# Kernel optimization log

Measured on AMD Instinct MI355X. Metric: run time of the kernel, lower is better.

Reference implementation:

```python
import jax, jax.numpy as jnp
import numpy as np

N_EMITTERS = 200000
N_FRAMES = 500


def setup_inputs() -> dict:
    key = jax.random.key(0)
    k1, _ = jax.random.split(key)
    # initial state must be one-hot per emitter: column 0 = 'on', column 1 = 'off'
    on = jax.random.bernoulli(k1, 0.5, (N_EMITTERS,))
    initial = jnp.stack([on, ~on], axis=-1).astype(jnp.float32)  # [N, 2] one-hot
    # transition[j] is the categorical distribution over {stay-ish, flip-ish} given row j
    transition = jnp.array([[0.5, 0.5], [0.9, 0.1]], dtype=jnp.float32)
    # transition_matrix[0] = identity (keep state), transition_matrix[1] = swap (flip state)
    transition_matrix = jnp.array([[[1.0, 0.0], [0.0, 1.0]],
                                   [[0.0, 1.0], [1.0, 0.0]]], dtype=jnp.float32)
    return {"initial": initial, "transition": transition,
            "transition_matrix": transition_matrix, "n_frames": N_FRAMES}


def reference(initial, transition, transition_matrix, n_frames):
    # Faithful translation of the per-frame Python loop as a single lax.scan.
    # Original: A = Cat(transition).sample([N]) -> A[n, j] ~ Cat(transition[j, :]) in {0, 1}
    #           t = (state * A).sum(-1)   (selects A at the current one-hot state index)
    #           state = state @ transition_matrix[t]
    # Output: per-frame on-mask (original returned np.where(state[:, 0] == 1) indices,
    # which has data-dependent shape; we return the equivalent dense mask).
    p1 = transition[:, 1]  # prob of drawing class 1 for each of the 2 row-distributions
    keys = jax.random.split(jax.random.key(42), n_frames)

    def step(state, k):
        u = jax.random.uniform(k, (state.shape[0], 2), dtype=state.dtype)  # [N, 2]
        A = (u < p1[None, :]).astype(state.dtype)  # categorical sample per row dist, {0,1}
        t = jnp.sum(state * A, axis=-1).astype(jnp.int32)  # [N] chosen action per emitter
        m = transition_matrix[t]  # [N, 2, 2] identity-or-swap
        new_state = jnp.einsum('ni,nij->nj', state, m)  # [N, 2] one-hot update
        return new_state, new_state[:, 0]

    _, on_mask = jax.lax.scan(step, initial, keys)
    return on_mask  # [n_frames, N], 1.0 where emitter is in the 'on' state
```

## Files before the change

kernel.cpp:

```cpp
#include <hip/hip_runtime.h>
#include <stdint.h>


#define ROTL32(x, d) __builtin_amdgcn_alignbit((x), (x), 32 - (d))

__device__ __forceinline__ void tf2x32(uint32_t k0, uint32_t k1,
                                       uint32_t x0, uint32_t x1,
                                       uint32_t& o0, uint32_t& o1) {
  const uint32_t k2 = k0 ^ k1 ^ 0x1BD11BDAu;
  x0 += k0; x1 += k1;
#define TF_R(d) { x0 += x1; x1 = ROTL32(x1, d) ^ x0; }
  TF_R(13) TF_R(15) TF_R(26) TF_R(6)
  x0 += k1; x1 += k2 + 1u;
  TF_R(17) TF_R(29) TF_R(16) TF_R(24)
  x0 += k2; x1 += k0 + 2u;
  TF_R(13) TF_R(15) TF_R(26) TF_R(6)
  x0 += k0; x1 += k1 + 3u;
  TF_R(17) TF_R(29) TF_R(16) TF_R(24)
  x0 += k1; x1 += k2 + 4u;
  TF_R(13) TF_R(15) TF_R(26) TF_R(6)
  x0 += k2; x1 += k0 + 5u;
#undef TF_R
  o0 = x0; o1 = x1;
}

__global__ void subkeys_kernel(uint2* __restrict__ ks, int nf, int cap) {
  const int f = blockIdx.x * blockDim.x + threadIdx.x;
  if (f < nf) {
    uint32_t a, b;
    tf2x32(0u, 42u, 0u, (uint32_t)f, a, b);
    ks[f] = make_uint2(a, b);
  } else if (f < cap) {
    ks[f] = make_uint2(0u, 0u);
  }
}

__device__ __forceinline__ uint32_t cipher(uint32_t k0, uint32_t k1,
                                           uint32_t k2, uint32_t c1,
                                           uint32_t c2, uint32_t c3,
                                           uint32_t c4, uint32_t c5,
                                           uint32_t x1in) {
  uint32_t x0 = k0 + x1in;
  uint32_t x1 = ROTL32(x1in, 13) ^ x0;
  x0 += x1; x1 = ROTL32(x1, 15) ^ x0;
  x0 += x1; x1 = ROTL32(x1, 26) ^ x0;
  x0 += x1; x1 = ROTL32(x1,  6) ^ x0;
  x1 += c1; x0 = x0 + k1 + x1;
  x1 = ROTL32(x1, 17) ^ x0;
  x0 += x1; x1 = ROTL32(x1, 29) ^ x0;
  x0 += x1; x1 = ROTL32(x1, 16) ^ x0;
  x0 += x1; x1 = ROTL32(x1, 24) ^ x0;
  x1 += c2; x0 = x0 + k2 + x1;
  x1 = ROTL32(x1, 13) ^ x0;
  x0 += x1; x1 = ROTL32(x1, 15) ^ x0;
  x0 += x1; x1 = ROTL32(x1, 26) ^ x0;
  x0 += x1; x1 = ROTL32(x1,  6) ^ x0;
  x1 += c3; x0 = x0 + k0 + x1;
  x1 = ROTL32(x1, 17) ^ x0;
  x0 += x1; x1 = ROTL32(x1, 29) ^ x0;
  x0 += x1; x1 = ROTL32(x1, 16) ^ x0;
  x0 += x1; x1 = ROTL32(x1, 24) ^ x0;
  x1 += c4; x0 = x0 + k1 + x1;
  x1 = ROTL32(x1, 13) ^ x0;
  x0 += x1; x1 = ROTL32(x1, 15) ^ x0;
  x0 += x1; x1 = ROTL32(x1, 26) ^ x0;
  x0 += x1; x1 = ROTL32(x1,  6) ^ x0;
  return (x0 + k2) ^ (x1 + c5);
}

template <int NC>
__device__ __forceinline__ void run_nc(
    const uint2* __restrict__ ks, float* __restrict__ out,
    const uint32_t* __restrict__ base, const int* __restrict__ noff,
    uint32_t* __restrict__ s, int N, int nf,
    uint32_t tsh0, uint32_t tsh1, uint32_t sw0, uint32_t sw1) {
  uint32_t thr[NC];
#pragma unroll
  for (int j = 0; j < NC; ++j) thr[j] = s[j] ? tsh1 : tsh0;

  const int ng = nf / 4;
  for (int g = 0; g < ng; ++g) {
    const int f0 = 4 * g;
    uint2 k[4];
#pragma unroll
    for (int i = 0; i < 4; ++i) k[i] = ks[f0 + i];

    uint32_t vals[4][NC];
#pragma unroll
    for (int i = 0; i < 4; ++i) {
      const uint32_t k0 = k[i].x, k1 = k[i].y;
      const uint32_t k2 = k0 ^ k1 ^ 0x1BD11BDAu;
      const uint32_t c1 = k2 + 1u, c2 = k0 + 2u, c3 = k1 + 3u,
                     c4 = k2 + 4u, c5 = k0 + 5u;
#pragma unroll
      for (int j = 0; j < NC; ++j) {
        const uint32_t r = cipher(k0, k1, k2, c1, c2, c3, c4, c5,
                                  base[j] + s[j] + k1);
        s[j] ^= (r < thr[j]) ? sw1 : sw0;
        thr[j] = s[j] ? tsh1 : tsh0;
        vals[i][j] = s[j] ? 0u : 0x3f800000u;
      }
    }
#pragma unroll
    for (int i = 0; i < 4; ++i) {
      uint32_t* row = (uint32_t*)out + (size_t)(f0 + i) * N;
#pragma unroll
      for (int j = 0; j < NC; ++j)
        __builtin_nontemporal_store(vals[i][j], row + noff[j]);
    }
  }
  for (int f = ng * 4; f < nf; ++f) {
    const uint2 kk = ks[f];
    const uint32_t k0 = kk.x, k1 = kk.y;
    const uint32_t k2 = k0 ^ k1 ^ 0x1BD11BDAu;
    const uint32_t c1 = k2 + 1u, c2 = k0 + 2u, c3 = k1 + 3u,
                   c4 = k2 + 4u, c5 = k0 + 5u;
    uint32_t* row = (uint32_t*)out + (size_t)f * N;
#pragma unroll
    for (int j = 0; j < NC; ++j) {
      const uint32_t r = cipher(k0, k1, k2, c1, c2, c3, c4, c5,
                                base[j] + s[j] + k1);
      s[j] ^= (r < thr[j]) ? sw1 : sw0;
      thr[j] = s[j] ? tsh1 : tsh0;
      __builtin_nontemporal_store(s[j] ? 0u : 0x3f800000u, row + noff[j]);
    }
  }
}

__device__ __forceinline__ void get_params(
    const float* transition, const float* tmat,
    uint32_t& tsh0, uint32_t& tsh1, uint32_t& sw0, uint32_t& sw1) {
  const uint64_t t0w = ((uint64_t)(uint32_t)ceilf(transition[1] * 8388608.0f)) << 9;
  const uint64_t t1w = ((uint64_t)(uint32_t)ceilf(transition[3] * 8388608.0f)) << 9;
  tsh0 = (t0w > 0xFFFFFFFFull) ? 0xFFFFFFFFu : (uint32_t)t0w;
  tsh1 = (t1w > 0xFFFFFFFFull) ? 0xFFFFFFFFu : (uint32_t)t1w;
  sw0 = (tmat[1] != 0.0f) ? 1u : 0u;
  sw1 = (tmat[5] != 0.0f) ? 1u : 0u;
}

__global__ __launch_bounds__(256) void markov3_kernel(
    const float* __restrict__ initial, const float* __restrict__ transition,
    const float* __restrict__ tmat, const uint2* __restrict__ ks,
    float* __restrict__ out, int N, int nf, int T, int extra) {
  const int t = blockIdx.x * blockDim.x + threadIdx.x;

  uint32_t tsh0, tsh1, sw0, sw1;
  get_params(transition, tmat, tsh0, tsh1, sw0, sw1);

  const int n0 = 3 * t;
  uint32_t s[4];
  uint32_t base[4];
  int noff[4];
#pragma unroll
  for (int j = 0; j < 3; ++j) {
    const int n = n0 + j;
    s[j] = (initial[2 * n] != 0.0f) ? 0u : 1u;
    base[j] = 2u * (uint32_t)n;
    noff[j] = n;
  }
  if (t < extra) {
    const int n3 = 3 * T + t;
    s[3] = (initial[2 * n3] != 0.0f) ? 0u : 1u;
    base[3] = 2u * (uint32_t)n3;
    noff[3] = n3;
    run_nc<4>(ks, out, base, noff, s, N, nf, tsh0, tsh1, sw0, sw1);
  } else {
    run_nc<3>(ks, out, base, noff, s, N, nf, tsh0, tsh1, sw0, sw1);
  }
}

__global__ __launch_bounds__(256) void markov_generic_kernel(
    const float* __restrict__ initial, const float* __restrict__ transition,
    const float* __restrict__ tmat, const uint2* __restrict__ ks,
    float* __restrict__ out, int N, int nf) {
  const int n = blockIdx.x * blockDim.x + threadIdx.x;
  if (n >= N) return;
  uint32_t tsh0, tsh1, sw0, sw1;
  get_params(transition, tmat, tsh0, tsh1, sw0, sw1);
  uint32_t s[1] = {(initial[2 * n] != 0.0f) ? 0u : 1u};
  uint32_t base[1] = {2u * (uint32_t)n};
  int noff[1] = {n};
  run_nc<1>(ks, out, base, noff, s, N, nf, tsh0, tsh1, sw0, sw1);
}

__global__ __launch_bounds__(256) void markov_lds_kernel(
    const float* __restrict__ initial, const float* __restrict__ transition,
    const float* __restrict__ tmat, float* __restrict__ out,
    int N, int nf, int cap) {
  extern __shared__ uint2 kf[];
  for (int f = threadIdx.x; f < cap; f += blockDim.x) {
    uint2 k = make_uint2(0u, 0u);
    if (f < nf) {
      uint32_t a, b;
      tf2x32(0u, 42u, 0u, (uint32_t)f, a, b);
      k = make_uint2(a, b);
    }
    kf[f] = k;
  }
  __syncthreads();
  const int n = blockIdx.x * blockDim.x + threadIdx.x;
  if (n >= N) return;
  uint32_t tsh0, tsh1, sw0, sw1;
  get_params(transition, tmat, tsh0, tsh1, sw0, sw1);
  uint32_t s[1] = {(initial[2 * n] != 0.0f) ? 0u : 1u};
  uint32_t base[1] = {2u * (uint32_t)n};
  int noff[1] = {n};
  run_nc<1>(kf, out, base, noff, s, N, nf, tsh0, tsh1, sw0, sw1);
}

extern "C" void kernel_launch(void* const* d_in, const int* in_sizes, int n_in,
                              void* d_out, int out_size, void* d_ws, size_t ws_size,
                              hipStream_t stream) {
  const float* initial    = (const float*)d_in[0];
  const float* transition = (const float*)d_in[1];
  const float* tmat       = (const float*)d_in[2];
  float* out = (float*)d_out;

  const int N  = in_sizes[0] / 2;
  const int nf = (N > 0) ? (out_size / N) : 0;
  if (N <= 0 || nf <= 0) return;

  const int cap = ((nf + 3) / 4 + 1) * 4;
  const size_t need = (size_t)cap * sizeof(uint2);

  if (ws_size < need) {
    const int block = 256;
    const int grid = (N + block - 1) / block;
    markov_lds_kernel<<<grid, block, need, stream>>>(initial, transition,
                                                     tmat, out, N, nf, cap);
    return;
  }

  uint2* ks = (uint2*)d_ws;
  subkeys_kernel<<<(cap + 255) / 256, 256, 0, stream>>>(ks, nf, cap);

  const int T = 65536;
  if (N >= 3 * T && N < 4 * T) {
    const int extra = N - 3 * T;
    markov3_kernel<<<T / 256, 256, 0, stream>>>(initial, transition, tmat,
                                                ks, out, N, nf, T, extra);
  } else {
    const int block = 256;
    const int grid = (N + block - 1) / block;
    markov_generic_kernel<<<grid, block, 0, stream>>>(initial, transition,
                                                      tmat, ks, out, N, nf);
  }
}
```

Measured before the change: 276.1 us.

## Stage 16-frame output tiles in LDS and write 128-bit nontemporal stores

Replaces the 3-4 emitters-per-thread kernel with a one-emitter-per-thread kernel. Each thread computes 16 frames into a double-buffered LDS tile, and the block then transposes the tile so each lane writes four contiguous floats with a 128-bit nontemporal store. The aim is to cut store instruction count and improve write coalescing for the 400 MB output. In exchange it adds a __syncthreads per 16 frames and LDS traffic, and it changes the parallelism from 65536 threads with 3 emitters each to 200000 threads with 1 each.

```diff
diff --git a/kernel.cpp b/kernel.cpp
--- a/kernel.cpp
+++ b/kernel.cpp
@@ -3,6 +3,8 @@
 
 
 #define ROTL32(x, d) __builtin_amdgcn_alignbit((x), (x), 32 - (d))
+
+typedef uint32_t v4u __attribute__((ext_vector_type(4)));
 
 __device__ __forceinline__ void tf2x32(uint32_t k0, uint32_t k1,
                                        uint32_t x0, uint32_t x1,
@@ -68,65 +70,6 @@
   return (x0 + k2) ^ (x1 + c5);
 }
 
-template <int NC>
-__device__ __forceinline__ void run_nc(
-    const uint2* __restrict__ ks, float* __restrict__ out,
-    const uint32_t* __restrict__ base, const int* __restrict__ noff,
-    uint32_t* __restrict__ s, int N, int nf,
-    uint32_t tsh0, uint32_t tsh1, uint32_t sw0, uint32_t sw1) {
-  uint32_t thr[NC];
-#pragma unroll
-  for (int j = 0; j < NC; ++j) thr[j] = s[j] ? tsh1 : tsh0;
-
-  const int ng = nf / 4;
-  for (int g = 0; g < ng; ++g) {
-    const int f0 = 4 * g;
-    uint2 k[4];
-#pragma unroll
-    for (int i = 0; i < 4; ++i) k[i] = ks[f0 + i];
-
-    uint32_t vals[4][NC];
-#pragma unroll
-    for (int i = 0; i < 4; ++i) {
-      const uint32_t k0 = k[i].x, k1 = k[i].y;
-      const uint32_t k2 = k0 ^ k1 ^ 0x1BD11BDAu;
-      const uint32_t c1 = k2 + 1u, c2 = k0 + 2u, c3 = k1 + 3u,
-                     c4 = k2 + 4u, c5 = k0 + 5u;
-#pragma unroll
-      for (int j = 0; j < NC; ++j) {
-        const uint32_t r = cipher(k0, k1, k2, c1, c2, c3, c4, c5,
-                                  base[j] + s[j] + k1);
-        s[j] ^= (r < thr[j]) ? sw1 : sw0;
-        thr[j] = s[j] ? tsh1 : tsh0;
-        vals[i][j] = s[j] ? 0u : 0x3f800000u;
-      }
-    }
-#pragma unroll
-    for (int i = 0; i < 4; ++i) {
-      uint32_t* row = (uint32_t*)out + (size_t)(f0 + i) * N;
-#pragma unroll
-      for (int j = 0; j < NC; ++j)
-        __builtin_nontemporal_store(vals[i][j], row + noff[j]);
-    }
-  }
-  for (int f = ng * 4; f < nf; ++f) {
-    const uint2 kk = ks[f];
-    const uint32_t k0 = kk.x, k1 = kk.y;
-    const uint32_t k2 = k0 ^ k1 ^ 0x1BD11BDAu;
-    const uint32_t c1 = k2 + 1u, c2 = k0 + 2u, c3 = k1 + 3u,
-                   c4 = k2 + 4u, c5 = k0 + 5u;
-    uint32_t* row = (uint32_t*)out + (size_t)f * N;
-#pragma unroll
-    for (int j = 0; j < NC; ++j) {
-      const uint32_t r = cipher(k0, k1, k2, c1, c2, c3, c4, c5,
-                                base[j] + s[j] + k1);
-      s[j] ^= (r < thr[j]) ? sw1 : sw0;
-      thr[j] = s[j] ? tsh1 : tsh0;
-      __builtin_nontemporal_store(s[j] ? 0u : 0x3f800000u, row + noff[j]);
-    }
-  }
-}
-
 __device__ __forceinline__ void get_params(
     const float* transition, const float* tmat,
     uint32_t& tsh0, uint32_t& tsh1, uint32_t& sw0, uint32_t& sw1) {
@@ -138,34 +81,76 @@
   sw1 = (tmat[5] != 0.0f) ? 1u : 0u;
 }
 
-__global__ __launch_bounds__(256) void markov3_kernel(
+__global__ __launch_bounds__(256) void markov_t_kernel(
     const float* __restrict__ initial, const float* __restrict__ transition,
     const float* __restrict__ tmat, const uint2* __restrict__ ks,
-    float* __restrict__ out, int N, int nf, int T, int extra) {
-  const int t = blockIdx.x * blockDim.x + threadIdx.x;
+    float* __restrict__ out, int N, int nf) {
+  __shared__ uint32_t buf[2][16 * 256];
+
+  const int t = (int)threadIdx.x;
+  const int n0b = (int)blockIdx.x * 256;
+  const int n = n0b + t;
+  const int rem = N - n0b;
+  const int valid = rem < 256 ? rem : 256;
+  const bool active = (t < valid);
 
   uint32_t tsh0, tsh1, sw0, sw1;
   get_params(transition, tmat, tsh0, tsh1, sw0, sw1);
 
-  const int n0 = 3 * t;
-  uint32_t s[4];
-  uint32_t base[4];
-  int noff[4];
+  uint32_t s = 0u, thr = tsh0, base = 0u;
+  if (active) {
+    s = (initial[2 * n] != 0.0f) ? 0u : 1u;
+    thr = s ? tsh1 : tsh0;
+    base = 2u * (uint32_t)n;
+  }
+
+  const int w = t >> 6, l = t & 63;
+  const int e0 = 4 * l;
+
+  const int ng = nf / 16;
+  for (int g = 0; g < ng; ++g) {
+    const int f0 = g * 16;
+    uint32_t* b = buf[g & 1];
+    if (active) {
 #pragma unroll
-  for (int j = 0; j < 3; ++j) {
-    const int n = n0 + j;
-    s[j] = (initial[2 * n] != 0.0f) ? 0u : 1u;
-    base[j] = 2u * (uint32_t)n;
-    noff[j] = n;
-  }
-  if (t < extra) {
-    const int n3 = 3 * T + t;
-    s[3] = (initial[2 * n3] != 0.0f) ? 0u : 1u;
-    base[3] = 2u * (uint32_t)n3;
-    noff[3] = n3;
-    run_nc<4>(ks, out, base, noff, s, N, nf, tsh0, tsh1, sw0, sw1);
-  } else {
-    run_nc<3>(ks, out, base, noff, s, N, nf, tsh0, tsh1, sw0, sw1);
+      for (int i = 0; i < 16; ++i) {
+        const uint2 kk = ks[f0 + i];
+        const uint32_t k0 = kk.x, k1 = kk.y;
+        const uint32_t k2 = k0 ^ k1 ^ 0x1BD11BDAu;
+        const uint32_t c1 = k2 + 1u, c2 = k0 + 2u, c3 = k1 + 3u,
+                       c4 = k2 + 4u, c5 = k0 + 5u;
+        const uint32_t r = cipher(k0, k1, k2, c1, c2, c3, c4, c5,
+                                  base + s + k1);
+        s ^= (r < thr) ? sw1 : sw0;
+        thr = s ? tsh1 : tsh0;
+        b[i * 256 + t] = s ? 0u : 0x3f800000u;
+      }
+    }
+    __syncthreads();
+    if (e0 < valid) {
+#pragma unroll
+      for (int c = 0; c < 4; ++c) {
+        const int r = 4 * w + c;
+        const v4u v = *(const v4u*)&b[r * 256 + e0];
+        __builtin_nontemporal_store(
+            v, (v4u*)(out + (size_t)(f0 + r) * N + (n0b + e0)));
+      }
+    }
+  }
+  for (int f = ng * 16; f < nf; ++f) {
+    if (active) {
+      const uint2 kk = ks[f];
+      const uint32_t k0 = kk.x, k1 = kk.y;
+      const uint32_t k2 = k0 ^ k1 ^ 0x1BD11BDAu;
+      const uint32_t c1 = k2 + 1u, c2 = k0 + 2u, c3 = k1 + 3u,
+                     c4 = k2 + 4u, c5 = k0 + 5u;
+      const uint32_t r = cipher(k0, k1, k2, c1, c2, c3, c4, c5,
+                                base + s + k1);
+      s ^= (r < thr) ? sw1 : sw0;
+      thr = s ? tsh1 : tsh0;
+      __builtin_nontemporal_store(s ? 0u : 0x3f800000u,
+                                  (uint32_t*)(out + (size_t)f * N) + n);
+    }
   }
 }
 
@@ -177,10 +162,21 @@
   if (n >= N) return;
   uint32_t tsh0, tsh1, sw0, sw1;
   get_params(transition, tmat, tsh0, tsh1, sw0, sw1);
-  uint32_t s[1] = {(initial[2 * n] != 0.0f) ? 0u : 1u};
-  uint32_t base[1] = {2u * (uint32_t)n};
-  int noff[1] = {n};
-  run_nc<1>(ks, out, base, noff, s, N, nf, tsh0, tsh1, sw0, sw1);
+  uint32_t s = (initial[2 * n] != 0.0f) ? 0u : 1u;
+  uint32_t thr = s ? tsh1 : tsh0;
+  const uint32_t base = 2u * (uint32_t)n;
+  for (int f = 0; f < nf; ++f) {
+    const uint2 kk = ks[f];
+    const uint32_t k0 = kk.x, k1 = kk.y;
+    const uint32_t k2 = k0 ^ k1 ^ 0x1BD11BDAu;
+    const uint32_t c1 = k2 + 1u, c2 = k0 + 2u, c3 = k1 + 3u,
+                   c4 = k2 + 4u, c5 = k0 + 5u;
+    const uint32_t r = cipher(k0, k1, k2, c1, c2, c3, c4, c5, base + s + k1);
+    s ^= (r < thr) ? sw1 : sw0;
+    thr = s ? tsh1 : tsh0;
+    __builtin_nontemporal_store(s ? 0u : 0x3f800000u,
+                                (uint32_t*)(out + (size_t)f * N) + n);
+  }
 }
 
 __global__ __launch_bounds__(256) void markov_lds_kernel(
@@ -202,10 +198,21 @@
   if (n >= N) return;
   uint32_t tsh0, tsh1, sw0, sw1;
   get_params(transition, tmat, tsh0, tsh1, sw0, sw1);
-  uint32_t s[1] = {(initial[2 * n] != 0.0f) ? 0u : 1u};
-  uint32_t base[1] = {2u * (uint32_t)n};
-  int noff[1] = {n};
-  run_nc<1>(kf, out, base, noff, s, N, nf, tsh0, tsh1, sw0, sw1);
+  uint32_t s = (initial[2 * n] != 0.0f) ? 0u : 1u;
+  uint32_t thr = s ? tsh1 : tsh0;
+  const uint32_t base = 2u * (uint32_t)n;
+  for (int f = 0; f < nf; ++f) {
+    const uint2 kk = kf[f];
+    const uint32_t k0 = kk.x, k1 = kk.y;
+    const uint32_t k2 = k0 ^ k1 ^ 0x1BD11BDAu;
+    const uint32_t c1 = k2 + 1u, c2 = k0 + 2u, c3 = k1 + 3u,
+                   c4 = k2 + 4u, c5 = k0 + 5u;
+    const uint32_t r = cipher(k0, k1, k2, c1, c2, c3, c4, c5, base + s + k1);
+    s ^= (r < thr) ? sw1 : sw0;
+    thr = s ? tsh1 : tsh0;
+    __builtin_nontemporal_store(s ? 0u : 0x3f800000u,
+                                (uint32_t*)(out + (size_t)f * N) + n);
+  }
 }
 
 extern "C" void kernel_launch(void* const* d_in, const int* in_sizes, int n_in,
@@ -220,12 +227,13 @@
   const int nf = (N > 0) ? (out_size / N) : 0;
   if (N <= 0 || nf <= 0) return;
 
-  const int cap = ((nf + 3) / 4 + 1) * 4;
+  const int block = 256;
+  const int grid = (N + block - 1) / block;
+
+  const int cap = ((nf + 15) / 16 + 1) * 16;
   const size_t need = (size_t)cap * sizeof(uint2);
 
   if (ws_size < need) {
-    const int block = 256;
-    const int grid = (N + block - 1) / block;
     markov_lds_kernel<<<grid, block, need, stream>>>(initial, transition,
                                                      tmat, out, N, nf, cap);
     return;
@@ -234,14 +242,10 @@
   uint2* ks = (uint2*)d_ws;
   subkeys_kernel<<<(cap + 255) / 256, 256, 0, stream>>>(ks, nf, cap);
 
-  const int T = 65536;
-  if (N >= 3 * T && N < 4 * T) {
-    const int extra = N - 3 * T;
-    markov3_kernel<<<T / 256, 256, 0, stream>>>(initial, transition, tmat,
-                                                ks, out, N, nf, T, extra);
+  if ((N % 4) == 0) {
+    markov_t_kernel<<<grid, block, 0, stream>>>(initial, transition, tmat,
+                                                ks, out, N, nf);
   } else {
-    const int block = 256;
-    const int grid = (N + block - 1) / block;
     markov_generic_kernel<<<grid, block, 0, stream>>>(initial, transition,
                                                       tmat, ks, out, N, nf);
   }
```

After: 272.2 us. No clear change (-1.4%).
